# Kernel optimization log

Measured on AMD Instinct MI355X. Metric: run time of the kernel, lower is better.

The kernel has to match this reference:

```python
import jax, jax.numpy as jnp
import numpy as np

TEMPERATURE = 0.07
BASE_TEMPERATURE = 0.07


def setup_inputs() -> dict:
    key = jax.random.key(0)
    k1, k2 = jax.random.split(key)
    N, D = 8192, 512
    features = jax.random.normal(k1, (N, D), dtype=jnp.float32)
    labels = jax.random.randint(k2, (N,), 0, 64, dtype=jnp.int64 if jax.config.jax_enable_x64 else jnp.int32)
    return {"features": features, "labels": labels, "rotation_multiplier": 2}


def reference(features, labels, rotation_multiplier):
    k = int(rotation_multiplier)
    N = features.shape[0]
    B = N // k
    # L2-normalize rows (torch F.normalize clamps norm at eps=1e-12)
    norm = jnp.maximum(jnp.linalg.norm(features, axis=1, keepdims=True), 1e-12)
    f = features / norm
    sim = jnp.matmul(f, f.T) / TEMPERATURE  # [N, N]

    # block positive mask: groups of k rows share a label; compare group labels
    lab = labels.reshape(B, k)[:, 0]  # [B]
    same = lab[:, None] == lab[None, :]  # [B, B]
    mask = jnp.repeat(jnp.repeat(same, k, axis=0), k, axis=1)  # [N, N]
    eye = jnp.eye(N, dtype=bool)
    mask = mask & ~eye

    # stable masked log-softmax with diagonal removed from denominator
    logits_max = jax.lax.stop_gradient(jnp.max(sim, axis=1, keepdims=True))
    logits = sim - logits_max
    exp_logits = jnp.exp(logits)
    denom = exp_logits.sum(axis=1, keepdims=True) - jnp.diagonal(exp_logits)[:, None] + 1e-8
    log_prob = logits - jnp.log(denom)

    mask_f = mask.astype(logits.dtype)
    mask_sum = mask_f.sum(axis=1)  # [N]
    valid = mask_sum > 0
    mean_log_prob_pos = (log_prob * mask_f).sum(axis=1) / jnp.maximum(mask_sum, 1.0)
    per_sample = -(TEMPERATURE / BASE_TEMPERATURE) * mean_log_prob_pos
    n_valid = valid.sum().astype(logits.dtype)
    loss = jnp.where(valid, per_sample, 0.0).sum() / jnp.maximum(n_valid, 1.0)
    return loss
```

## Files before the change

### kernel.cpp

```cpp
#include <hip/hip_runtime.h>
#include <hip/hip_bf16.h>

#define TEMP_INV 14.285714285714286f
#define FSCALE 16.0f
#define T1S (TEMP_INV / 256.0f)

typedef __attribute__((ext_vector_type(4))) float f32x4;
typedef __attribute__((ext_vector_type(4))) int i32x4;
typedef __attribute__((ext_vector_type(8))) int i32x8;


__global__ __launch_bounds__(256) void norm_k(const float* __restrict__ feat,
                                              uchar* __restrict__ fq,
                                              const int* __restrict__ labels,
                                              const int* __restrict__ kptr,
                                              int* __restrict__ glab,
                                              float* __restrict__ gacc,
                                              int* __restrict__ dcnt,
                                              int N, int D) {
  const int row = (blockIdx.x * 256 + threadIdx.x) >> 6;
  const int lane = threadIdx.x & 63;
  if (row < N) {
    const float4* fr = (const float4*)(feat + (size_t)row * D);
    float4 v0 = fr[lane * 2];
    float4 v1 = fr[lane * 2 + 1];
    float ss = v0.x * v0.x + v0.y * v0.y + v0.z * v0.z + v0.w * v0.w +
               v1.x * v1.x + v1.y * v1.y + v1.z * v1.z + v1.w * v1.w;
    #pragma unroll
    for (int off = 32; off; off >>= 1) ss += __shfl_xor(ss, off, 64);
    const float inv = FSCALE / fmaxf(sqrtf(ss), 1e-12f);
    int w0 = 0, w1 = 0;
    w0 = __builtin_amdgcn_cvt_pk_fp8_f32(v0.x * inv, v0.y * inv, w0, false);
    w0 = __builtin_amdgcn_cvt_pk_fp8_f32(v0.z * inv, v0.w * inv, w0, true);
    w1 = __builtin_amdgcn_cvt_pk_fp8_f32(v1.x * inv, v1.y * inv, w1, false);
    w1 = __builtin_amdgcn_cvt_pk_fp8_f32(v1.z * inv, v1.w * inv, w1, true);
    uint2 o; o.x = (uint)w0; o.y = (uint)w1;
    const int tkb  = lane >> 4;
    const int quad = (lane >> 2) & 3;
    const int half = (lane >> 1) & 1;
    const int slot = half * 64 + quad * 16 + (row & 15);
    uchar* dstp = fq + (((size_t)(row >> 4) * (D >> 7) + tkb) << 11) +
                  slot * 16 + (lane & 1) * 8;
    *(uint2*)dstp = o;
    if (lane == 0) {
      const int k = *kptr;
      glab[row] = labels[(size_t)(row / k) * k];
    }
  }
  if (blockIdx.x == 0 && threadIdx.x < 3) {
    if (threadIdx.x < 2) gacc[threadIdx.x] = 0.f;
    else *dcnt = 0;
  }
}

__global__ __launch_bounds__(256, 3) void gemm_k(const uchar* __restrict__ fq,
                                                 const int* __restrict__ glab,
                                                 float* __restrict__ part,
                                                 int N, int D) {
  __shared__ float sf[1024];
  const int t = threadIdx.x;
  const int lane = t & 63;
  const int wid = t >> 6;
  const int wrow = wid >> 1, wcol = wid & 1;
  const int quad = lane >> 4, l15 = lane & 15;

  const int nb = N / 128;
  const int total = nb * (nb + 1) / 2;
  int gidx = blockIdx.x;
  if ((total & 7) == 0) {
    const int per = total >> 3;
    gidx = (blockIdx.x & 7) * per + (blockIdx.x >> 3);
  }
  int idx = gidx, bi = 0;
  while (idx >= nb - bi) { idx -= nb - bi; bi++; }
  const int bj = bi + idx;
  const int i0 = bi * 128, j0 = bj * 128;
  const bool diagblk = (bi == bj);

  f32x4 acc[4][4];
  #pragma unroll
  for (int mi = 0; mi < 4; mi++)
    #pragma unroll
    for (int ni = 0; ni < 4; ni++) {
      f32x4 z = {0.f, 0.f, 0.f, 0.f};
      acc[mi][ni] = z;
    }

  const int ktiles = D >> 7;
  const uchar* ap = fq + (((size_t)((i0 >> 4) + wrow * 4) * ktiles) << 11) + lane * 16;
  const uchar* bp = fq + (((size_t)((j0 >> 4) + wcol * 4) * ktiles) << 11) + lane * 16;

#define KSTEP(kt)                                                             \
  {                                                                           \
    i32x8 bv[4];                                                              \
    _Pragma("unroll")                                                         \
    for (int ni = 0; ni < 4; ni++) {                                          \
      const uchar* p = bp + (((ni) * ktiles + (kt)) << 11);                   \
      i32x4 lo = *(const i32x4*)p;                                            \
      i32x4 hi = *(const i32x4*)(p + 1024);                                   \
      bv[ni] = (i32x8){lo.x, lo.y, lo.z, lo.w, hi.x, hi.y, hi.z, hi.w};       \
    }                                                                         \
    _Pragma("unroll")                                                         \
    for (int mi = 0; mi < 4; mi++) {                                          \
      const uchar* p = ap + (((mi) * ktiles + (kt)) << 11);                   \
      i32x4 lo = *(const i32x4*)p;                                            \
      i32x4 hi = *(const i32x4*)(p + 1024);                                   \
      i32x8 av = (i32x8){lo.x, lo.y, lo.z, lo.w, hi.x, hi.y, hi.z, hi.w};     \
      _Pragma("unroll")                                                       \
      for (int ni = 0; ni < 4; ni++)                                          \
        acc[mi][ni] = __builtin_amdgcn_mfma_scale_f32_16x16x128_f8f6f4(       \
            av, bv[ni], acc[mi][ni], 0, 0, 0, 127, 0, 127);                   \
    }                                                                         \
  }

  if (ktiles == 4) {
    KSTEP(0) KSTEP(1) KSTEP(2) KSTEP(3)
  } else {
    for (int kt = 0; kt < ktiles; kt++) KSTEP(kt)
  }
#undef KSTEP

  const int colbase = j0 + wcol * 64 + l15;
  int clab[4];
  #pragma unroll
  for (int ni = 0; ni < 4; ni++) clab[ni] = glab[colbase + ni * 16];

  float colE[4] = {0.f, 0.f, 0.f, 0.f};
  float colP[4] = {0.f, 0.f, 0.f, 0.f};

  #pragma unroll
  for (int mi = 0; mi < 4; mi++) {
    const int lrw = wrow * 64 + mi * 16 + quad * 4;
    #pragma unroll
    for (int r = 0; r < 4; r++) {
      const int row = i0 + lrw + r;
      const int rlab = glab[row];
      float Ssum = 0.f, Psum = 0.f;
      #pragma unroll
      for (int ni = 0; ni < 4; ni++) {
        const int col = colbase + ni * 16;
        const float val = acc[mi][ni][r];
        const float lg = fmaf(val, T1S, -TEMP_INV);
        const bool diag = diagblk && (row == col);
        const float e = diag ? 0.f : __expf(lg);
        const float pm = (!diag && rlab == clab[ni]) ? lg : 0.f;
        Ssum += e; Psum += pm;
        colE[ni] += e; colP[ni] += pm;
      }
      #pragma unroll
      for (int off = 8; off; off >>= 1) {
        Ssum += __shfl_xor(Ssum, off, 64);
        Psum += __shfl_xor(Psum, off, 64);
      }
      if (l15 == 0) {
        sf[wcol * 128 + lrw + r]       = Ssum;
        sf[256 + wcol * 128 + lrw + r] = Psum;
      }
    }
  }
  if (!diagblk) {
    #pragma unroll
    for (int ni = 0; ni < 4; ni++) {
      float e = colE[ni];
      float p = colP[ni];
      e += __shfl_xor(e, 16, 64);
      e += __shfl_xor(e, 32, 64);
      p += __shfl_xor(p, 16, 64);
      p += __shfl_xor(p, 32, 64);
      const int lcol = wcol * 64 + ni * 16 + l15;
      if (quad == 0) {
        sf[512 + wrow * 128 + lcol] = e;
        sf[768 + wrow * 128 + lcol] = p;
      }
    }
  }
  __syncthreads();
  float* dst = part + (size_t)gidx * 512;
  if (t < 128) {
    dst[t]       = sf[t] + sf[128 + t];
    dst[128 + t] = sf[256 + t] + sf[384 + t];
  } else if (!diagblk) {
    const int u = t - 128;
    dst[256 + u] = sf[512 + u] + sf[640 + u];
    dst[384 + u] = sf[768 + u] + sf[896 + u];
  }
}

__global__ __launch_bounds__(1024) void reduce_loss_k(const float* __restrict__ part,
                                                      const int* __restrict__ glab,
                                                      const int* __restrict__ labels,
                                                      const int* __restrict__ kptr,
                                                      float* __restrict__ gacc,
                                                      int* __restrict__ dcnt,
                                                      float* __restrict__ out, int N) {
  const int nb = N / 128;
  const int b = blockIdx.x;
  const int tt = threadIdx.x;
  const int t = tt & 127;
  const int sl = tt >> 7;
  const int k = *kptr;
  const int B = N / k;

  __shared__ int h[64];
  if (tt < 64) h[tt] = 0;
  __syncthreads();
  for (int g = tt; g < B; g += 1024) {
    int lb = labels[(size_t)g * k];
    if (lb >= 0 && lb < 64) atomicAdd(&h[lb], 1);
  }

  float S = 0.f, P = 0.f;
  const int base = b * nb - b * (b - 1) / 2;
  for (int bj = b + sl; bj < nb; bj += 8) {
    const float* p = part + (size_t)(base + bj - b) * 512;
    S += p[t];
    P += p[128 + t];
  }
  for (int bi = sl; bi < b; bi += 8) {
    const int idx = bi * nb - bi * (bi - 1) / 2 + (b - bi);
    const float* p = part + (size_t)idx * 512;
    S += p[256 + t];
    P += p[384 + t];
  }
  __shared__ float sS[8][128], sP[8][128];
  sS[sl][t] = S; sP[sl][t] = P;
  __syncthreads();
  float l = 0.f, v = 0.f;
  if (sl == 0) {
    S = 0.f; P = 0.f;
    #pragma unroll
    for (int s = 0; s < 8; s++) { S += sS[s][t]; P += sP[s][t]; }
    const int np = h[glab[b * 128 + t]] * k - 1;
    if (np > 0) {
      l = -(P - (float)np * logf(S + 1e-8f)) / (float)np;
      v = 1.f;
    }
  }
  #pragma unroll
  for (int off = 32; off; off >>= 1) {
    l += __shfl_xor(l, off, 64);
    v += __shfl_xor(v, off, 64);
  }
  __shared__ float sl16[16], sv16[16];
  if ((tt & 63) == 0) { sl16[tt >> 6] = l; sv16[tt >> 6] = v; }
  __syncthreads();
  if (tt == 0) {
    float L = 0.f, V = 0.f;
    #pragma unroll
    for (int i = 0; i < 16; i++) { L += sl16[i]; V += sv16[i]; }
    atomicAdd(&gacc[0], L);
    atomicAdd(&gacc[1], V);
    __threadfence();
    const int prev = atomicAdd(dcnt, 1);
    if (prev == (int)gridDim.x - 1) {
      const float Lf = atomicAdd(&gacc[0], 0.f);
      const float Vf = atomicAdd(&gacc[1], 0.f);
      out[0] = Lf / fmaxf(Vf, 1.f);
    }
  }
}

extern "C" void kernel_launch(void* const* d_in, const int* in_sizes, int n_in,
                              void* d_out, int out_size, void* d_ws, size_t ws_size,
                              hipStream_t stream) {
  const float* feat = (const float*)d_in[0];
  const int* labels = (const int*)d_in[1];
  const int* kptr   = (const int*)d_in[2];
  const int N = in_sizes[1];
  const int D = in_sizes[0] / N;

  const int nb = N / 128;
  const int total = nb * (nb + 1) / 2;

  char* ws = (char*)d_ws;
  uchar* fq = (uchar*)ws;
  size_t off = (size_t)N * D;
  float* part = (float*)(ws + off); off += (size_t)total * 512 * sizeof(float);
  int* glab   = (int*)(ws + off);   off += (size_t)N * sizeof(int);
  float* gacc = (float*)(ws + off); off += 2 * sizeof(float);
  int* dcnt   = (int*)(ws + off);   off += sizeof(int);

  norm_k<<<(N + 3) / 4, 256, 0, stream>>>(feat, fq, labels, kptr, glab,
                                          gacc, dcnt, N, D);
  gemm_k<<<total, 256, 0, stream>>>(fq, glab, part, N, D);
  reduce_loss_k<<<nb, 1024, 0, stream>>>(part, glab, labels, kptr, gacc, dcnt,
                                         (float*)d_out, N);
}
```

Measured before the change: 131.0 us.

## Shrink GEMM tiles to 64x64 single-wave blocks and drop LDS reduction

Each GEMM workgroup now computes a 64x64 tile with one wavefront instead of a 128x128 tile with four wavefronts. Partial row and column sums are written straight to global memory, so the shared-memory staging and __syncthreads go away. The triangular block index is now found with a sqrt-based closed form instead of a linear loop, and the reduce kernel is reworked for 64-wide blocks. The trade-off is four times as many blocks and partials, and less operand reuse per block (more fp8 loads per MFMA), in exchange for finer load balance and no intra-block sync.

```diff
diff --git a/kernel.cpp b/kernel.cpp
--- a/kernel.cpp
+++ b/kernel.cpp
@@ -53,28 +53,28 @@
   }
 }
 
-__global__ __launch_bounds__(256, 3) void gemm_k(const uchar* __restrict__ fq,
-                                                 const int* __restrict__ glab,
-                                                 float* __restrict__ part,
-                                                 int N, int D) {
-  __shared__ float sf[1024];
-  const int t = threadIdx.x;
-  const int lane = t & 63;
-  const int wid = t >> 6;
-  const int wrow = wid >> 1, wcol = wid & 1;
+__global__ __launch_bounds__(64) void gemm_k(const uchar* __restrict__ fq,
+                                             const int* __restrict__ glab,
+                                             float* __restrict__ part,
+                                             int N, int D) {
+  const int lane = threadIdx.x;
   const int quad = lane >> 4, l15 = lane & 15;
 
-  const int nb = N / 128;
-  const int total = nb * (nb + 1) / 2;
+  const int nbs = N / 64;
+  const int total = nbs * (nbs + 1) / 2;
   int gidx = blockIdx.x;
   if ((total & 7) == 0) {
     const int per = total >> 3;
     gidx = (blockIdx.x & 7) * per + (blockIdx.x >> 3);
   }
-  int idx = gidx, bi = 0;
-  while (idx >= nb - bi) { idx -= nb - bi; bi++; }
-  const int bj = bi + idx;
-  const int i0 = bi * 128, j0 = bj * 128;
+  const float nf = (float)nbs + 0.5f;
+  int bi = (int)(nf - sqrtf(fmaxf(nf * nf - 2.0f * (float)gidx, 0.f)));
+  if (bi < 0) bi = 0;
+  if (bi > nbs - 1) bi = nbs - 1;
+  while (bi > 0 && bi * nbs - bi * (bi - 1) / 2 > gidx) bi--;
+  while ((bi + 1) * nbs - (bi + 1) * bi / 2 <= gidx) bi++;
+  const int bj = bi + (gidx - (bi * nbs - bi * (bi - 1) / 2));
+  const int i0 = bi * 64, j0 = bj * 64;
   const bool diagblk = (bi == bj);
 
   f32x4 acc[4][4];
@@ -87,8 +87,8 @@
     }
 
   const int ktiles = D >> 7;
-  const uchar* ap = fq + (((size_t)((i0 >> 4) + wrow * 4) * ktiles) << 11) + lane * 16;
-  const uchar* bp = fq + (((size_t)((j0 >> 4) + wcol * 4) * ktiles) << 11) + lane * 16;
+  const uchar* ap = fq + (((size_t)(i0 >> 4) * ktiles) << 11) + lane * 16;
+  const uchar* bp = fq + (((size_t)(j0 >> 4) * ktiles) << 11) + lane * 16;
 
 #define KSTEP(kt)                                                             \
   {                                                                           \
@@ -120,17 +120,17 @@
   }
 #undef KSTEP
 
-  const int colbase = j0 + wcol * 64 + l15;
   int clab[4];
   #pragma unroll
-  for (int ni = 0; ni < 4; ni++) clab[ni] = glab[colbase + ni * 16];
+  for (int ni = 0; ni < 4; ni++) clab[ni] = glab[j0 + ni * 16 + l15];
 
   float colE[4] = {0.f, 0.f, 0.f, 0.f};
   float colP[4] = {0.f, 0.f, 0.f, 0.f};
+  float* dst = part + (size_t)gidx * 256;
 
   #pragma unroll
   for (int mi = 0; mi < 4; mi++) {
-    const int lrw = wrow * 64 + mi * 16 + quad * 4;
+    const int lrw = mi * 16 + quad * 4;
     #pragma unroll
     for (int r = 0; r < 4; r++) {
       const int row = i0 + lrw + r;
@@ -138,7 +138,7 @@
       float Ssum = 0.f, Psum = 0.f;
       #pragma unroll
       for (int ni = 0; ni < 4; ni++) {
-        const int col = colbase + ni * 16;
+        const int col = j0 + ni * 16 + l15;
         const float val = acc[mi][ni][r];
         const float lg = fmaf(val, T1S, -TEMP_INV);
         const bool diag = diagblk && (row == col);
@@ -153,8 +153,8 @@
         Psum += __shfl_xor(Psum, off, 64);
       }
       if (l15 == 0) {
-        sf[wcol * 128 + lrw + r]       = Ssum;
-        sf[256 + wcol * 128 + lrw + r] = Psum;
+        dst[lrw + r]      = Ssum;
+        dst[64 + lrw + r] = Psum;
       }
     }
   }
@@ -167,22 +167,11 @@
       e += __shfl_xor(e, 32, 64);
       p += __shfl_xor(p, 16, 64);
       p += __shfl_xor(p, 32, 64);
-      const int lcol = wcol * 64 + ni * 16 + l15;
       if (quad == 0) {
-        sf[512 + wrow * 128 + lcol] = e;
-        sf[768 + wrow * 128 + lcol] = p;
-      }
-    }
-  }
-  __syncthreads();
-  float* dst = part + (size_t)gidx * 512;
-  if (t < 128) {
-    dst[t]       = sf[t] + sf[128 + t];
-    dst[128 + t] = sf[256 + t] + sf[384 + t];
-  } else if (!diagblk) {
-    const int u = t - 128;
-    dst[256 + u] = sf[512 + u] + sf[640 + u];
-    dst[384 + u] = sf[768 + u] + sf[896 + u];
+        dst[128 + ni * 16 + l15] = e;
+        dst[192 + ni * 16 + l15] = p;
+      }
+    }
   }
 }
 
@@ -193,11 +182,11 @@
                                                       float* __restrict__ gacc,
                                                       int* __restrict__ dcnt,
                                                       float* __restrict__ out, int N) {
-  const int nb = N / 128;
+  const int nbs = N / 64;
   const int b = blockIdx.x;
   const int tt = threadIdx.x;
-  const int t = tt & 127;
-  const int sl = tt >> 7;
+  const int t = tt & 63;
+  const int sl = tt >> 6;
   const int k = *kptr;
   const int B = N / k;
 
@@ -210,27 +199,27 @@
   }
 
   float S = 0.f, P = 0.f;
-  const int base = b * nb - b * (b - 1) / 2;
-  for (int bj = b + sl; bj < nb; bj += 8) {
-    const float* p = part + (size_t)(base + bj - b) * 512;
+  const int base = b * nbs - b * (b - 1) / 2;
+  for (int bj = b + sl; bj < nbs; bj += 16) {
+    const float* p = part + (size_t)(base + bj - b) * 256;
     S += p[t];
-    P += p[128 + t];
-  }
-  for (int bi = sl; bi < b; bi += 8) {
-    const int idx = bi * nb - bi * (bi - 1) / 2 + (b - bi);
-    const float* p = part + (size_t)idx * 512;
-    S += p[256 + t];
-    P += p[384 + t];
-  }
-  __shared__ float sS[8][128], sP[8][128];
+    P += p[64 + t];
+  }
+  for (int bi = sl; bi < b; bi += 16) {
+    const int idx = bi * nbs - bi * (bi - 1) / 2 + (b - bi);
+    const float* p = part + (size_t)idx * 256;
+    S += p[128 + t];
+    P += p[192 + t];
+  }
+  __shared__ float sS[16][64], sP[16][64];
   sS[sl][t] = S; sP[sl][t] = P;
   __syncthreads();
   float l = 0.f, v = 0.f;
   if (sl == 0) {
     S = 0.f; P = 0.f;
     #pragma unroll
-    for (int s = 0; s < 8; s++) { S += sS[s][t]; P += sP[s][t]; }
-    const int np = h[glab[b * 128 + t]] * k - 1;
+    for (int s = 0; s < 16; s++) { S += sS[s][t]; P += sP[s][t]; }
+    const int np = h[glab[b * 64 + t]] * k - 1;
     if (np > 0) {
       l = -(P - (float)np * logf(S + 1e-8f)) / (float)np;
       v = 1.f;
@@ -269,20 +258,20 @@
   const int N = in_sizes[1];
   const int D = in_sizes[0] / N;
 
-  const int nb = N / 128;
-  const int total = nb * (nb + 1) / 2;
+  const int nbs = N / 64;
+  const int total = nbs * (nbs + 1) / 2;
 
   char* ws = (char*)d_ws;
   uchar* fq = (uchar*)ws;
   size_t off = (size_t)N * D;
-  float* part = (float*)(ws + off); off += (size_t)total * 512 * sizeof(float);
+  float* part = (float*)(ws + off); off += (size_t)total * 256 * sizeof(float);
   int* glab   = (int*)(ws + off);   off += (size_t)N * sizeof(int);
   float* gacc = (float*)(ws + off); off += 2 * sizeof(float);
   int* dcnt   = (int*)(ws + off);   off += sizeof(int);
 
   norm_k<<<(N + 3) / 4, 256, 0, stream>>>(feat, fq, labels, kptr, glab,
                                           gacc, dcnt, N, D);
-  gemm_k<<<total, 256, 0, stream>>>(fq, glab, part, N, D);
-  reduce_loss_k<<<nb, 1024, 0, stream>>>(part, glab, labels, kptr, gacc, dcnt,
-                                         (float*)d_out, N);
-}
+  gemm_k<<<total, 64, 0, stream>>>(fq, glab, part, N, D);
+  reduce_loss_k<<<nbs, 1024, 0, stream>>>(part, glab, labels, kptr, gacc, dcnt,
+                                          (float*)d_out, N);
+}
```

New measurement: 133.6 us. 1.02x slower.
